# Kernel tuning notes

Measured on AMD Instinct MI355X. Metric: run time of the kernel, lower is better.

The kernel has to match this reference:

```python
import jax, jax.numpy as jnp
import numpy as np

N_NODES = 100000
N_EDGES = 3200000
IN_FEATS = 256
OUT_FEATS = 128
N_LAYERS = 3


def setup_inputs() -> dict:
    key = jax.random.key(0)
    k1, k2, k3, k4, k5, k6 = jax.random.split(key, 6)
    x = jax.random.normal(k1, (N_NODES, IN_FEATS), dtype=jnp.float32)
    row = jax.random.randint(k2, (N_EDGES,), 0, N_NODES, dtype=jnp.int64)
    col = jax.random.randint(k3, (N_EDGES,), 0, N_NODES, dtype=jnp.int64)
    vals = jax.random.uniform(k4, (N_EDGES,), dtype=jnp.float32)
    W = jax.random.normal(k5, (OUT_FEATS, IN_FEATS), dtype=jnp.float32) * (1.0 / np.sqrt(IN_FEATS))
    b = jax.random.normal(k6, (OUT_FEATS,), dtype=jnp.float32) * 0.01
    return {"x": x, "row": row, "col": col, "vals": vals, "W": W, "b": b, "n_layers": N_LAYERS}


def reference(x, row, col, vals, W, b, n_layers):
    n_nodes = x.shape[0]
    # z = linear(x)
    z = jnp.einsum('ni,oi->no', x, W) + b  # [N, out_feats]
    # repeated SpMM: z_new[r] = sum over edges e with row[e]==r of vals[e] * z[col[e]]
    for _ in range(int(n_layers)):
        gathered = vals[:, None] * z[col]  # [E, out_feats]
        z = jax.ops.segment_sum(gathered, row, num_segments=n_nodes)
    return z
```

## Files before the change

kernel.cpp:

```cpp
#include <hip/hip_runtime.h>
#include <hip/hip_bf16.h>

#define NNODES   100000
#define INF      256
#define OUTF     128
#define NLAYERS  3

#define RPB   196
#define NBKT  511
#define CAP   7168
#define EPB   4096

typedef unsigned short u16;

typedef __attribute__((ext_vector_type(8))) __bf16 bf16x8;
typedef __attribute__((ext_vector_type(4))) float  f32x4;

__device__ __forceinline__ float bf2f(u16 u) {
    union { unsigned int i; float f; } c; c.i = ((unsigned int)u) << 16; return c.f;
}
__device__ __forceinline__ u16 f2bf(float f) {
    union { float f; unsigned int i; } c; c.f = f;
    unsigned int lsb = (c.i >> 16) & 1;
    return (u16)((c.i + 0x7FFF + lsb) >> 16);
}

__global__ __launch_bounds__(256) void partition_kernel(
    const int* __restrict__ row, const int* __restrict__ col,
    const float* __restrict__ vals, int* __restrict__ alloc,
    int2* __restrict__ epart, int E)
{
    __shared__ int srow[EPB];
    __shared__ int hist[NBKT];
    __shared__ int gbase[NBKT];
    int tid = threadIdx.x;
    int e0  = blockIdx.x * EPB;

    for (int i = tid; i < NBKT; i += 256) hist[i] = 0;
    __syncthreads();
    for (int i = tid; i < EPB; i += 256) {
        int e = e0 + i;
        int r = (e < E) ? row[e] : -1;
        srow[i] = r;
        if (r >= 0) atomicAdd(&hist[r / RPB], 1);
    }
    __syncthreads();
    for (int i = tid; i < NBKT; i += 256) {
        int c = hist[i];
        gbase[i] = c ? atomicAdd(&alloc[i], c) : 0;
    }
    __syncthreads();
    for (int i = tid; i < NBKT; i += 256) hist[i] = 0;
    __syncthreads();
    for (int i = tid; i < EPB; i += 256) {
        int r = srow[i];
        if (r >= 0) {
            int b    = r / RPB;
            int lofs = atomicAdd(&hist[b], 1);
            int pos  = gbase[b] + lofs;
            int e    = e0 + i;
            epart[(size_t)b * CAP + pos] =
                make_int2(col[e] | ((r - b * RPB) << 17), __float_as_int(vals[e]));
        }
    }
}

__global__ __launch_bounds__(256) void bucket_scatter_kernel(
    const int* __restrict__ alloc, int2* __restrict__ epart,
    int* __restrict__ rowptr, int* __restrict__ rowcnt, int M)
{
    int b = blockIdx.x;
    int n = alloc[b];
    int2* src = epart + (size_t)b * CAP;
    __shared__ int2 stage[CAP];
    __shared__ int  hist[256];
    __shared__ int  excl[256];
    __shared__ int  wofs[RPB];
    int tid = threadIdx.x;

    for (int i = tid; i < n; i += 256) stage[i] = src[i];
    hist[tid] = 0;
    __syncthreads();
    for (int i = tid; i < n; i += 256) atomicAdd(&hist[stage[i].x >> 17], 1);
    __syncthreads();
    int v = hist[tid];
    excl[tid] = v;
    __syncthreads();
    for (int off = 1; off < 256; off <<= 1) {
        int t = (tid >= off) ? excl[tid - off] : 0;
        __syncthreads();
        excl[tid] += t;
        __syncthreads();
    }
    int ex = excl[tid] - v;
    int r  = b * RPB + tid;
    if (tid < RPB && r < M) {
        rowptr[r] = b * CAP + ex;
        rowcnt[r] = v;
    }
    if (tid < RPB) wofs[tid] = ex;
    __syncthreads();
    for (int i = tid; i < n; i += 256) {
        int2 p  = stage[i];
        int  rl = p.x >> 17;
        int  pos = atomicAdd(&wofs[rl], 1);
        src[pos] = make_int2(p.x & 0x1FFFF, p.y);
    }
}

__global__ __launch_bounds__(256) void gemm_mfma_kernel(
    const float* __restrict__ x, const float* __restrict__ W,
    const float* __restrict__ b, u16* __restrict__ z, int M)
{
    __shared__ __align__(16) u16 Wl[128 * 256];
    int tid  = threadIdx.x;
    int lane = tid & 63;
    int wv   = tid >> 6;

    {
        int c  = tid >> 1;
        int k0 = (tid & 1) * 128;
        const float* src = W + (size_t)c * INF + k0;
        u16* dst = Wl + c * 256;
        int swz = (c & 7) << 3;
#pragma unroll
        for (int t = 0; t < 32; ++t) {
            float4 a = ((const float4*)src)[t];
            int k = (k0 + 4 * t) ^ swz;
            dst[k + 0] = f2bf(a.x); dst[k + 1] = f2bf(a.y);
            dst[k + 2] = f2bf(a.z); dst[k + 3] = f2bf(a.w);
        }
    }

    int cl = lane & 15;
    int g  = lane >> 4;
    float bo[8];
#pragma unroll
    for (int f = 0; f < 8; ++f) bo[f] = b[16 * f + cl];

    __syncthreads();

    int n0 = blockIdx.x * 64 + wv * 16;
    int nr = n0 + cl;
    if (nr >= M) nr = M - 1;
    const float* xrow = x + (size_t)nr * INF + 8 * g;

    f32x4 acc[8];
#pragma unroll
    for (int f = 0; f < 8; ++f) {
        f32x4 a; a[0] = bo[f]; a[1] = bo[f]; a[2] = bo[f]; a[3] = bo[f];
        acc[f] = a;
    }

#pragma unroll
    for (int ks = 0; ks < 8; ++ks) {
        int k0 = ks * 32;
        float4 a0 = ((const float4*)(xrow + k0))[0];
        float4 a1 = ((const float4*)(xrow + k0))[1];
        bf16x8 af;
        af[0] = (__bf16)a0.x; af[1] = (__bf16)a0.y;
        af[2] = (__bf16)a0.z; af[3] = (__bf16)a0.w;
        af[4] = (__bf16)a1.x; af[5] = (__bf16)a1.y;
        af[6] = (__bf16)a1.z; af[7] = (__bf16)a1.w;
#pragma unroll
        for (int f = 0; f < 8; ++f) {
            int c  = 16 * f + cl;
            int ke = (k0 + 8 * g) ^ ((c & 7) << 3);
            bf16x8 bfr = *(const bf16x8*)(Wl + c * 256 + ke);
            acc[f] = __builtin_amdgcn_mfma_f32_16x16x32_bf16(af, bfr, acc[f], 0, 0, 0);
        }
    }

    int rbase = n0 + 4 * g;
#pragma unroll
    for (int j = 0; j < 4; ++j) {
        int n = rbase + j;
        if (n < M) {
            u16* zr = z + (size_t)n * OUTF;
#pragma unroll
            for (int f = 0; f < 8; ++f)
                zr[16 * f + cl] = f2bf(acc[f][j]);
        }
    }
}

template <bool MASKED>
__device__ __forceinline__ void edge8(const int2* __restrict__ ep, int e, int end,
                                      const u16* __restrict__ zin, int f,
                                      float2* __restrict__ acc) {
    int2 p[8];
#pragma unroll
    for (int i = 0; i < 8; ++i) {
        int idx = MASKED ? ((e + i < end) ? e + i : end - 1) : (e + i);
        p[i] = ep[idx];
    }
    ushort2 zb[8];
#pragma unroll
    for (int i = 0; i < 8; ++i)
        zb[i] = *(const ushort2*)(zin + (size_t)p[i].x * OUTF + f);
#pragma unroll
    for (int i = 0; i < 8; ++i) {
        float v = __int_as_float(p[i].y);
        if (MASKED) v = (e + i < end) ? v : 0.f;
        acc[i & 3].x += v * bf2f(zb[i].x);
        acc[i & 3].y += v * bf2f(zb[i].y);
    }
}

template <bool OUT_BF16>
__global__ __launch_bounds__(256) void spmm_kernel(const int* __restrict__ rowptr,
                                                   const int* __restrict__ rowcnt,
                                                   const int2* __restrict__ epart,
                                                   const u16* __restrict__ zin,
                                                   void* __restrict__ zout, int M) {
    int r = blockIdx.x * 4 + (threadIdx.x >> 6);
    if (r >= M) return;
    int lane = threadIdx.x & 63;
    int f    = lane * 2;

    int start = __builtin_amdgcn_readfirstlane(rowptr[r]);
    int n     = __builtin_amdgcn_readfirstlane(rowcnt[r]);
    int end   = start + n;

    float2 acc[4] = {{0.f,0.f},{0.f,0.f},{0.f,0.f},{0.f,0.f}};
    int e = start;
    for (; e + 8 <= end; e += 8) edge8<false>(epart, e, end, zin, f, acc);
    if (e < end)                 edge8<true >(epart, e, end, zin, f, acc);

    float sx = (acc[0].x + acc[1].x) + (acc[2].x + acc[3].x);
    float sy = (acc[0].y + acc[1].y) + (acc[2].y + acc[3].y);
    if (OUT_BF16) {
        ushort2 o; o.x = f2bf(sx); o.y = f2bf(sy);
        *(ushort2*)((u16*)zout + (size_t)r * OUTF + f) = o;
    } else {
        *(float2*)((float*)zout + (size_t)r * OUTF + f) = make_float2(sx, sy);
    }
}


extern "C" void kernel_launch(void* const* d_in, const int* in_sizes, int n_in,
                              void* d_out, int out_size, void* d_ws, size_t ws_size,
                              hipStream_t stream) {
    const float* x    = (const float*)d_in[0];
    const int*   row  = (const int*)d_in[1];
    const int*   col  = (const int*)d_in[2];
    const float* vals = (const float*)d_in[3];
    const float* W    = (const float*)d_in[4];
    const float* b    = (const float*)d_in[5];
    float* out = (float*)d_out;

    const int M = in_sizes[0] / INF;
    const int E = in_sizes[1];

    u16*   zb0    = (u16*)d_ws;
    u16*   zb1    = zb0 + (size_t)M * OUTF;
    int*   rowptr = (int*)(zb1 + (size_t)M * OUTF);
    int*   rowcnt = rowptr + M;
    int*   alloc  = rowcnt + M;
    size_t ofs = (size_t)((char*)(alloc + NBKT) - (char*)d_ws);
    ofs = (ofs + 7) & ~(size_t)7;
    int2*  epart  = (int2*)((char*)d_ws + ofs);

    hipMemsetAsync(alloc, 0, NBKT * sizeof(int), stream);
    partition_kernel<<<(E + EPB - 1) / EPB, 256, 0, stream>>>(row, col, vals, alloc, epart, E);
    bucket_scatter_kernel<<<NBKT, 256, 0, stream>>>(alloc, epart, rowptr, rowcnt, M);

    gemm_mfma_kernel<<<(M + 63) / 64, 256, 0, stream>>>(x, W, b, zb0, M);

    int sgrid = (M + 3) / 4;
    spmm_kernel<true ><<<sgrid, 256, 0, stream>>>(rowptr, rowcnt, epart, zb0, (void*)zb1, M);
    spmm_kernel<true ><<<sgrid, 256, 0, stream>>>(rowptr, rowcnt, epart, zb1, (void*)zb0, M);
    spmm_kernel<false><<<sgrid, 256, 0, stream>>>(rowptr, rowcnt, epart, zb0, (void*)out, M);
}
```

Measured before the change: 646.2 us.

## Vectorize partition loads, pre-convert W to bf16, unroll SpMM gather by 16

Several changes land together. The partition kernel doubles edges per block and reads row, col and vals as int4/float4, rereading row instead of staging it in shared memory. A new small kernel converts W to bf16 once, so each GEMM block copies bf16x8 vectors into LDS instead of converting floats itself. Row segments are padded to even length so 16-byte edge-pair loads stay aligned, and the SpMM main loop handles 16 edges per iteration with all index loads and then all gathers issued up front under sched_barrier to expose memory-level parallelism. The risks are higher register pressure in SpMM, an extra kernel launch, and a bucket overflow: padding can push a bucket's packed total past CAP, since the unpadded average is already about 6272 per bucket.

```diff
diff --git a/kernel.cpp b/kernel.cpp
--- a/kernel.cpp
+++ b/kernel.cpp
@@ -9,7 +9,7 @@
 #define RPB   196
 #define NBKT  511
 #define CAP   7168
-#define EPB   4096
+#define EPB   8192
 
 typedef unsigned short u16;
 
@@ -23,6 +23,15 @@
     union { float f; unsigned int i; } c; c.f = f;
     unsigned int lsb = (c.i >> 16) & 1;
     return (u16)((c.i + 0x7FFF + lsb) >> 16);
+}
+
+__global__ __launch_bounds__(256) void wconv_kernel(const float* __restrict__ W,
+                                                    u16* __restrict__ Wbf) {
+    int i = (blockIdx.x * 256 + threadIdx.x) * 4;
+    float4 a = *(const float4*)(W + i);
+    ushort4 o;
+    o.x = f2bf(a.x); o.y = f2bf(a.y); o.z = f2bf(a.z); o.w = f2bf(a.w);
+    *(ushort4*)(Wbf + i) = o;
 }
 
 __global__ __launch_bounds__(256) void partition_kernel(
@@ -30,7 +39,6 @@
     const float* __restrict__ vals, int* __restrict__ alloc,
     int2* __restrict__ epart, int E)
 {
-    __shared__ int srow[EPB];
     __shared__ int hist[NBKT];
     __shared__ int gbase[NBKT];
     int tid = threadIdx.x;
@@ -38,11 +46,15 @@
 
     for (int i = tid; i < NBKT; i += 256) hist[i] = 0;
     __syncthreads();
-    for (int i = tid; i < EPB; i += 256) {
+    for (int i = tid * 4; i < EPB; i += 1024) {
         int e = e0 + i;
-        int r = (e < E) ? row[e] : -1;
-        srow[i] = r;
-        if (r >= 0) atomicAdd(&hist[r / RPB], 1);
+        if (e < E) {
+            int4 r4 = *(const int4*)(row + e);
+            atomicAdd(&hist[r4.x / RPB], 1);
+            atomicAdd(&hist[r4.y / RPB], 1);
+            atomicAdd(&hist[r4.z / RPB], 1);
+            atomicAdd(&hist[r4.w / RPB], 1);
+        }
     }
     __syncthreads();
     for (int i = tid; i < NBKT; i += 256) {
@@ -52,15 +64,22 @@
     __syncthreads();
     for (int i = tid; i < NBKT; i += 256) hist[i] = 0;
     __syncthreads();
-    for (int i = tid; i < EPB; i += 256) {
-        int r = srow[i];
-        if (r >= 0) {
-            int b    = r / RPB;
-            int lofs = atomicAdd(&hist[b], 1);
-            int pos  = gbase[b] + lofs;
-            int e    = e0 + i;
-            epart[(size_t)b * CAP + pos] =
-                make_int2(col[e] | ((r - b * RPB) << 17), __float_as_int(vals[e]));
+    for (int i = tid * 4; i < EPB; i += 1024) {
+        int e = e0 + i;
+        if (e < E) {
+            int4   r4 = *(const int4*)(row + e);
+            int4   c4 = *(const int4*)(col + e);
+            float4 v4 = *(const float4*)(vals + e);
+            int   rr[4] = {r4.x, r4.y, r4.z, r4.w};
+            int   cc[4] = {c4.x, c4.y, c4.z, c4.w};
+            float vv[4] = {v4.x, v4.y, v4.z, v4.w};
+#pragma unroll
+            for (int t = 0; t < 4; ++t) {
+                int b    = rr[t] / RPB;
+                int lofs = atomicAdd(&hist[b], 1);
+                epart[(size_t)b * CAP + gbase[b] + lofs] =
+                    make_int2(cc[t] | ((rr[t] - b * RPB) << 17), __float_as_int(vv[t]));
+            }
         }
     }
 }
@@ -84,7 +103,8 @@
     for (int i = tid; i < n; i += 256) atomicAdd(&hist[stage[i].x >> 17], 1);
     __syncthreads();
     int v = hist[tid];
-    excl[tid] = v;
+    int w = (v + 1) & ~1;
+    excl[tid] = w;
     __syncthreads();
     for (int off = 1; off < 256; off <<= 1) {
         int t = (tid >= off) ? excl[tid - off] : 0;
@@ -92,7 +112,7 @@
         excl[tid] += t;
         __syncthreads();
     }
-    int ex = excl[tid] - v;
+    int ex = excl[tid] - w;
     int r  = b * RPB + tid;
     if (tid < RPB && r < M) {
         rowptr[r] = b * CAP + ex;
@@ -109,7 +129,7 @@
 }
 
 __global__ __launch_bounds__(256) void gemm_mfma_kernel(
-    const float* __restrict__ x, const float* __restrict__ W,
+    const float* __restrict__ x, const u16* __restrict__ Wbf,
     const float* __restrict__ b, u16* __restrict__ z, int M)
 {
     __shared__ __align__(16) u16 Wl[128 * 256];
@@ -118,17 +138,15 @@
     int wv   = tid >> 6;
 
     {
-        int c  = tid >> 1;
-        int k0 = (tid & 1) * 128;
-        const float* src = W + (size_t)c * INF + k0;
+        int c = tid >> 1;
+        int h = tid & 1;
+        const bf16x8* src = (const bf16x8*)(Wbf + c * 256 + h * 128);
         u16* dst = Wl + c * 256;
-        int swz = (c & 7) << 3;
-#pragma unroll
-        for (int t = 0; t < 32; ++t) {
-            float4 a = ((const float4*)src)[t];
-            int k = (k0 + 4 * t) ^ swz;
-            dst[k + 0] = f2bf(a.x); dst[k + 1] = f2bf(a.y);
-            dst[k + 2] = f2bf(a.z); dst[k + 3] = f2bf(a.w);
+        int swz = c & 7;
+#pragma unroll
+        for (int t = 0; t < 16; ++t) {
+            int j = h * 16 + t;
+            *(bf16x8*)(dst + 8 * (j ^ swz)) = src[t];
         }
     }
 
@@ -224,8 +242,29 @@
 
     float2 acc[4] = {{0.f,0.f},{0.f,0.f},{0.f,0.f},{0.f,0.f}};
     int e = start;
-    for (; e + 8 <= end; e += 8) edge8<false>(epart, e, end, zin, f, acc);
-    if (e < end)                 edge8<true >(epart, e, end, zin, f, acc);
+    for (; e + 16 <= end; e += 16) {
+        int4 q[8];
+#pragma unroll
+        for (int j = 0; j < 8; ++j) q[j] = *((const int4*)(epart + e) + j);
+        __builtin_amdgcn_sched_barrier(0);
+        ushort2 zb[16];
+#pragma unroll
+        for (int j = 0; j < 8; ++j) {
+            zb[2*j]   = *(const ushort2*)(zin + (size_t)q[j].x * OUTF + f);
+            zb[2*j+1] = *(const ushort2*)(zin + (size_t)q[j].z * OUTF + f);
+        }
+        __builtin_amdgcn_sched_barrier(0);
+#pragma unroll
+        for (int j = 0; j < 8; ++j) {
+            float v0 = __int_as_float(q[j].y);
+            float v1 = __int_as_float(q[j].w);
+            acc[(2*j)   & 3].x += v0 * bf2f(zb[2*j].x);
+            acc[(2*j)   & 3].y += v0 * bf2f(zb[2*j].y);
+            acc[(2*j+1) & 3].x += v1 * bf2f(zb[2*j+1].x);
+            acc[(2*j+1) & 3].y += v1 * bf2f(zb[2*j+1].y);
+        }
+    }
+    for (; e < end; e += 8) edge8<true>(epart, e, end, zin, f, acc);
 
     float sx = (acc[0].x + acc[1].x) + (acc[2].x + acc[3].x);
     float sy = (acc[0].y + acc[1].y) + (acc[2].y + acc[3].y);
@@ -257,15 +296,20 @@
     int*   rowptr = (int*)(zb1 + (size_t)M * OUTF);
     int*   rowcnt = rowptr + M;
     int*   alloc  = rowcnt + M;
-    size_t ofs = (size_t)((char*)(alloc + NBKT) - (char*)d_ws);
-    ofs = (ofs + 7) & ~(size_t)7;
-    int2*  epart  = (int2*)((char*)d_ws + ofs);
+    size_t wb_ofs = (size_t)((char*)(alloc + NBKT) - (char*)d_ws);
+    wb_ofs = (wb_ofs + 15) & ~(size_t)15;
+    u16*   Wbf    = (u16*)((char*)d_ws + wb_ofs);
+    size_t ep_ofs = wb_ofs + (size_t)OUTF * INF * sizeof(u16);
+    ep_ofs = (ep_ofs + 15) & ~(size_t)15;
+    int2*  epart  = (int2*)((char*)d_ws + ep_ofs);
+
+    wconv_kernel<<<(OUTF * INF) / 1024, 256, 0, stream>>>(W, Wbf);
 
     hipMemsetAsync(alloc, 0, NBKT * sizeof(int), stream);
     partition_kernel<<<(E + EPB - 1) / EPB, 256, 0, stream>>>(row, col, vals, alloc, epart, E);
     bucket_scatter_kernel<<<NBKT, 256, 0, stream>>>(alloc, epart, rowptr, rowcnt, M);
 
-    gemm_mfma_kernel<<<(M + 63) / 64, 256, 0, stream>>>(x, W, b, zb0, M);
+    gemm_mfma_kernel<<<(M + 63) / 64, 256, 0, stream>>>(x, Wbf, b, zb0, M);
 
     int sgrid = (M + 3) / 4;
     spmm_kernel<true ><<<sgrid, 256, 0, stream>>>(rowptr, rowcnt, epart, zb0, (void*)zb1, M);
```

Result: faster. 608.8 us (-5.8%).
